# Kernel optimization log

Measured on AMD Instinct MI355X. Metric: run time of the kernel, lower is better.

## Reference

```python
import jax, jax.numpy as jnp
import numpy as np

N_ENTITIES = 100000
D = 128
N_EDGES = 600000
N_RELATIONS = 32
N_USERS = 50000
NNZ = 1000000


def setup_inputs() -> dict:
    key = jax.random.key(0)
    k = jax.random.split(key, 7)
    entity_emb = jax.random.normal(k[0], (N_ENTITIES, D), dtype=jnp.float32)
    edge_index = jax.random.randint(k[1], (2, N_EDGES), 0, N_ENTITIES, dtype=jnp.int64)
    # edge_type in [1, N_RELATIONS] so that weight[edge_type - 1] is in-range
    edge_type = jax.random.randint(k[2], (N_EDGES,), 1, N_RELATIONS + 1, dtype=jnp.int64)
    interact_rows = jax.random.randint(k[3], (NNZ,), 0, N_USERS, dtype=jnp.int64)
    interact_cols = jax.random.randint(k[4], (NNZ,), 0, N_ENTITIES, dtype=jnp.int64)
    interact_vals = jax.random.uniform(k[5], (NNZ,), dtype=jnp.float32)
    weight = jax.random.normal(k[6], (N_RELATIONS, D), dtype=jnp.float32)
    return {
        "entity_emb": entity_emb,
        "edge_index": edge_index,
        "edge_type": edge_type,
        "interact_rows": interact_rows,
        "interact_cols": interact_cols,
        "interact_vals": interact_vals,
        "n_users": N_USERS,
        "weight": weight,
    }


def reference(entity_emb, edge_index, edge_type, interact_rows, interact_cols,
              interact_vals, n_users, weight):
    n_entities = entity_emb.shape[0]
    head, tail = edge_index[0], edge_index[1]

    # KG aggregate: gather -> elementwise mul -> scatter_mean over head
    edge_relation_emb = weight[edge_type - 1]              # [E, D]
    neigh_relation_emb = entity_emb[tail] * edge_relation_emb  # [E, D]
    seg_sum = jax.ops.segment_sum(neigh_relation_emb, head, num_segments=n_entities)
    counts = jax.ops.segment_sum(jnp.ones((head.shape[0],), dtype=entity_emb.dtype),
                                 head, num_segments=n_entities)
    entity_agg = seg_sum / jnp.maximum(counts, 1.0)[:, None]  # mean; empty rows -> 0

    # user aggregate: sparse (COO) @ dense  == segment-sum of scaled gathered rows
    gathered = interact_vals[:, None] * entity_emb[interact_cols]  # [nnz, D]
    user_agg = jax.ops.segment_sum(gathered, interact_rows, num_segments=n_users)

    return entity_agg, user_agg
```

## Files before the change

kernel.cpp:

```cpp
#include <hip/hip_runtime.h>

#define D 128

__device__ __forceinline__ float bf2f(unsigned short u) {
    union { unsigned int i; float f; } v;
    v.i = ((unsigned int)u) << 16;
    return v.f;
}
__device__ __forceinline__ unsigned short f2bf(float f) {
    union { float f; unsigned int i; } v;
    v.f = f;
    unsigned int x = v.i;
    unsigned int round_bit = (x >> 16) & 1u;
    x += 0x7fffu + round_bit;
    return (unsigned short)(x >> 16);
}

__global__ void detect_kernel(const int* __restrict__ et_i32,
                              const unsigned short* __restrict__ emb_u16,
                              int* __restrict__ flags) {
    int lane = threadIdx.x;
    int v = et_i32[2 * lane + 1];
    unsigned long long b_i64 = __ballot(v != 0);

    unsigned short a = emb_u16[2 * lane];
    unsigned short c = emb_u16[2 * lane + 1];
    int e1 = (a >> 7) & 0xFF;
    int e2 = (c >> 7) & 0xFF;
    unsigned long long b_f32 = __ballot(e1 > 140 || e2 > 140);

    if (lane == 0) {
        flags[0] = (b_i64 == 0ULL) ? 1 : 0;
        flags[1] = (b_f32 != 0ULL) ? 1 : 0;
    }
}

__device__ __forceinline__ int idx_at(const void* p, long long i, bool i64) {
    return i64 ? (int)((const long long*)p)[i] : ((const int*)p)[i];
}

__global__ void hist_all(const void* __restrict__ ei, const void* __restrict__ rows,
                         int* __restrict__ cnt, const int* __restrict__ flags,
                         int n_edges, int nnz, int n_entities) {
    long long i = (long long)blockIdx.x * blockDim.x + threadIdx.x;
    bool i64 = flags[0] != 0;
    if (i < n_edges) {
        atomicAdd(&cnt[idx_at(ei, i, i64)], 1);
    } else if (i < (long long)n_edges + nnz) {
        atomicAdd(&cnt[n_entities + idx_at(rows, i - n_edges, i64)], 1);
    }
}

__device__ __forceinline__ int block_scan_excl_256(int v, int* total) {
    __shared__ int tmp[256];
    int tid = threadIdx.x;
    tmp[tid] = v;
    __syncthreads();
    #pragma unroll
    for (int ofs = 1; ofs < 256; ofs <<= 1) {
        int t = (tid >= ofs) ? tmp[tid - ofs] : 0;
        __syncthreads();
        tmp[tid] += t;
        __syncthreads();
    }
    int incl = tmp[tid];
    *total = tmp[255];
    __syncthreads();
    return incl - v;
}

__global__ void scan_p1(const int* __restrict__ cnt, int* __restrict__ bsums, int n) {
    int i = blockIdx.x * 256 + threadIdx.x;
    int v = (i < n) ? cnt[i] : 0;
    int total;
    block_scan_excl_256(v, &total);
    if (threadIdx.x == 0) bsums[blockIdx.x] = total;
}

__global__ void scan_p2(int* __restrict__ bsums, int nb) {
    int tid = threadIdx.x;
    int chunk = (nb + 255) / 256;
    int beg = tid * chunk;
    int end = min(beg + chunk, nb);
    int s = 0;
    for (int i = beg; i < end; ++i) s += bsums[i];
    int total;
    int run = block_scan_excl_256(s, &total);
    for (int i = beg; i < end; ++i) {
        int c = bsums[i];
        bsums[i] = run;
        run += c;
    }
}

__global__ void scan_p3(int* __restrict__ cnt, const int* __restrict__ bsums,
                        int* __restrict__ off, int n) {
    int i = blockIdx.x * 256 + threadIdx.x;
    int v = (i < n) ? cnt[i] : 0;
    int total;
    int excl = block_scan_excl_256(v, &total);
    int base = bsums[blockIdx.x];
    if (i < n) {
        off[i] = base + excl;
        cnt[i] = 0;
        if (i == n - 1) off[n] = base + excl + v;
    }
}

__global__ void scatter_all(const void* __restrict__ ei, const void* __restrict__ et,
                            const void* __restrict__ rows, const void* __restrict__ cols,
                            const void* __restrict__ vals,
                            const int* __restrict__ off, int* __restrict__ cur,
                            int2* __restrict__ pairs, const int* __restrict__ flags,
                            int n_edges, int nnz, int n_entities) {
    long long i = (long long)blockIdx.x * blockDim.x + threadIdx.x;
    bool i64 = flags[0] != 0;
    if (i < n_edges) {
        int head = idx_at(ei, i, i64);
        int tail = idx_at(ei, (long long)n_edges + i, i64);
        int rel  = idx_at(et, i, i64) - 1;
        int pos = off[head] + atomicAdd(&cur[head], 1);
        int2 p; p.x = tail; p.y = rel;
        pairs[pos] = p;
    } else if (i < (long long)n_edges + nnz) {
        long long k = i - n_edges;
        bool f32 = flags[1] != 0;
        int rr = n_entities + idx_at(rows, k, i64);
        int c = idx_at(cols, k, i64);
        float v = f32 ? ((const float*)vals)[k] : bf2f(((const unsigned short*)vals)[k]);
        int pos = off[rr] + atomicAdd(&cur[rr], 1);
        int2 p; p.x = c; p.y = __float_as_int(v);
        pairs[pos] = p;
    }
}

__device__ __forceinline__ void unpack8(uint4 q, float* e) {
    e[0] = bf2f((unsigned short)(q.x & 0xFFFFu)); e[1] = bf2f((unsigned short)(q.x >> 16));
    e[2] = bf2f((unsigned short)(q.y & 0xFFFFu)); e[3] = bf2f((unsigned short)(q.y >> 16));
    e[4] = bf2f((unsigned short)(q.z & 0xFFFFu)); e[5] = bf2f((unsigned short)(q.z >> 16));
    e[6] = bf2f((unsigned short)(q.w & 0xFFFFu)); e[7] = bf2f((unsigned short)(q.w >> 16));
}

__global__ void agg_all(const void* __restrict__ emb, const void* __restrict__ weight,
                        const int* __restrict__ off, const int2* __restrict__ pairs,
                        void* __restrict__ out, const int* __restrict__ flags,
                        int n_entities, int n_total) {
    int gid = blockIdx.x * blockDim.x + threadIdx.x;
    int w = gid >> 6;
    int lane = gid & 63;
    if (w >= n_total) return;
    bool f32 = flags[1] != 0;
    bool isU = (w >= n_entities);
    int m = lane & 15;
    int g = lane >> 4;
    int beg = off[w], end = off[w + 1];

    float acc[8];
    #pragma unroll
    for (int i = 0; i < 8; ++i) acc[i] = 0.f;

    if (!f32) {
        const uint4* embq = (const uint4*)emb;
        if (isU) {
            for (int j = beg + g; j < end; j += 4) {
                int2 p = pairs[j];
                uint4 q = embq[(size_t)p.x * 16 + m];
                float v = __int_as_float(p.y);
                float e[8]; unpack8(q, e);
                #pragma unroll
                for (int i = 0; i < 8; ++i) acc[i] += v * e[i];
            }
        } else {
            const uint4* wq = (const uint4*)weight;
            for (int j = beg + g; j < end; j += 4) {
                int2 p = pairs[j];
                uint4 q  = embq[(size_t)p.x * 16 + m];
                uint4 qw = wq[(size_t)p.y * 16 + m];
                float e[8], wv[8]; unpack8(q, e); unpack8(qw, wv);
                #pragma unroll
                for (int i = 0; i < 8; ++i) acc[i] += e[i] * wv[i];
            }
        }
    } else {
        const float* embf = (const float*)emb;
        if (isU) {
            for (int j = beg + g; j < end; j += 4) {
                int2 p = pairs[j];
                const float4* rp = (const float4*)(embf + (size_t)p.x * D);
                float4 a = rp[m * 2], b = rp[m * 2 + 1];
                float v = __int_as_float(p.y);
                acc[0] += v * a.x; acc[1] += v * a.y; acc[2] += v * a.z; acc[3] += v * a.w;
                acc[4] += v * b.x; acc[5] += v * b.y; acc[6] += v * b.z; acc[7] += v * b.w;
            }
        } else {
            const float* wf = (const float*)weight;
            for (int j = beg + g; j < end; j += 4) {
                int2 p = pairs[j];
                const float4* rp = (const float4*)(embf + (size_t)p.x * D);
                const float4* wp = (const float4*)(wf + (size_t)p.y * D);
                float4 a = rp[m * 2], b = rp[m * 2 + 1];
                float4 wa = wp[m * 2], wb = wp[m * 2 + 1];
                acc[0] += a.x * wa.x; acc[1] += a.y * wa.y; acc[2] += a.z * wa.z; acc[3] += a.w * wa.w;
                acc[4] += b.x * wb.x; acc[5] += b.y * wb.y; acc[6] += b.z * wb.z; acc[7] += b.w * wb.w;
            }
        }
    }

    #pragma unroll
    for (int i = 0; i < 8; ++i) {
        acc[i] += __shfl_xor(acc[i], 16, 64);
        acc[i] += __shfl_xor(acc[i], 32, 64);
    }

    if (!isU) {
        float rcp = 1.0f / fmaxf((float)(end - beg), 1.0f);
        #pragma unroll
        for (int i = 0; i < 8; ++i) acc[i] *= rcp;
    }

    if (g == 0) {
        if (!f32) {
            uint4 o;
            o.x = (unsigned int)f2bf(acc[0]) | ((unsigned int)f2bf(acc[1]) << 16);
            o.y = (unsigned int)f2bf(acc[2]) | ((unsigned int)f2bf(acc[3]) << 16);
            o.z = (unsigned int)f2bf(acc[4]) | ((unsigned int)f2bf(acc[5]) << 16);
            o.w = (unsigned int)f2bf(acc[6]) | ((unsigned int)f2bf(acc[7]) << 16);
            ((uint4*)out)[(size_t)w * 16 + m] = o;
        } else {
            float4* rp = (float4*)((float*)out + (size_t)w * D);
            float4 a, b;
            a.x = acc[0]; a.y = acc[1]; a.z = acc[2]; a.w = acc[3];
            b.x = acc[4]; b.y = acc[5]; b.z = acc[6]; b.w = acc[7];
            rp[m * 2] = a;
            rp[m * 2 + 1] = b;
        }
    }
}

extern "C" void kernel_launch(void* const* d_in, const int* in_sizes, int n_in,
                              void* d_out, int out_size, void* d_ws, size_t ws_size,
                              hipStream_t stream) {
    const void* emb  = d_in[0];
    const void* ei   = d_in[1];
    const void* et   = d_in[2];
    const void* rows = d_in[3];
    const void* cols = d_in[4];
    const void* vals = d_in[5];

    const void* weight = d_in[n_in - 1];
    for (int i = n_in - 1; i >= 5; --i) {
        if (in_sizes[i] >= 256) { weight = d_in[i]; break; }
    }

    int n_entities = in_sizes[0] / D;
    int n_edges    = in_sizes[2];
    int nnz        = in_sizes[5];
    int n_users    = out_size / D - n_entities;

    int n_concat = n_entities + n_users;
    int nb = (n_concat + 255) / 256;

    char* p = (char*)d_ws;
    int2* pairs = (int2*)p;                      p += (size_t)(n_edges + nnz) * sizeof(int2);
    int*  off   = (int*)p;                       p += (size_t)(n_concat + 1) * sizeof(int);
    int*  cnt   = (int*)p;                       p += (size_t)n_concat * sizeof(int);
    int*  bsums = (int*)p;                       p += (size_t)nb * sizeof(int);
    int*  flags = (int*)p;

    (void)hipMemsetAsync(cnt, 0, (size_t)n_concat * sizeof(int), stream);

    const int tpb = 256;

    detect_kernel<<<1, 64, 0, stream>>>((const int*)et, (const unsigned short*)emb, flags);

    {
        long long n = (long long)n_edges + nnz;
        hist_all<<<(int)((n + tpb - 1) / tpb), tpb, 0, stream>>>(
            ei, rows, cnt, flags, n_edges, nnz, n_entities);
    }

    scan_p1<<<nb, 256, 0, stream>>>(cnt, bsums, n_concat);
    scan_p2<<<1, 256, 0, stream>>>(bsums, nb);
    scan_p3<<<nb, 256, 0, stream>>>(cnt, bsums, off, n_concat);

    {
        long long n = (long long)n_edges + nnz;
        scatter_all<<<(int)((n + tpb - 1) / tpb), tpb, 0, stream>>>(
            ei, et, rows, cols, vals, off, cnt, pairs, flags, n_edges, nnz, n_entities);
    }

    {
        long long threads = (long long)n_concat * 64;
        agg_all<<<(int)((threads + tpb - 1) / tpb), tpb, 0, stream>>>(
            emb, weight, off, pairs, d_out, flags, n_entities, n_concat);
    }
}
```

Measured before the change: 408.5 us.

## Record atomic ranks in histogram to skip scatter atomics; shuffle-broadcast pair indices

The histogram pass now keeps each element's destination and the rank returned by its atomicAdd, so the scatter pass writes every pair straight to off[dst]+rank with no second round of atomics. This only happens when the workspace can hold the extra rank array, otherwise the old scatter runs. The f32 aggregation path also loads up to 64 pairs coalesced in one go and broadcasts them with wave shuffles, instead of each lane group reading pairs one at a time. The cost is an extra 8-byte-per-element write and read, plus more branching in the aggregation kernel.

```diff
diff --git a/kernel.cpp b/kernel.cpp
--- a/kernel.cpp
+++ b/kernel.cpp
@@ -40,14 +40,19 @@
 }
 
 __global__ void hist_all(const void* __restrict__ ei, const void* __restrict__ rows,
-                         int* __restrict__ cnt, const int* __restrict__ flags,
+                         int* __restrict__ cnt, int2* __restrict__ dr,
+                         const int* __restrict__ flags,
                          int n_edges, int nnz, int n_entities) {
     long long i = (long long)blockIdx.x * blockDim.x + threadIdx.x;
     bool i64 = flags[0] != 0;
     if (i < n_edges) {
-        atomicAdd(&cnt[idx_at(ei, i, i64)], 1);
+        int dst = idx_at(ei, i, i64);
+        int r = atomicAdd(&cnt[dst], 1);
+        if (dr) { int2 p; p.x = dst; p.y = r; dr[i] = p; }
     } else if (i < (long long)n_edges + nnz) {
-        atomicAdd(&cnt[n_entities + idx_at(rows, i - n_edges, i64)], 1);
+        int dst = n_entities + idx_at(rows, i - n_edges, i64);
+        int r = atomicAdd(&cnt[dst], 1);
+        if (dr) { int2 p; p.x = dst; p.y = r; dr[i] = p; }
     }
 }
 
@@ -104,6 +109,30 @@
         off[i] = base + excl;
         cnt[i] = 0;
         if (i == n - 1) off[n] = base + excl + v;
+    }
+}
+
+__global__ void scatter_rank(const void* __restrict__ ei, const void* __restrict__ et,
+                             const void* __restrict__ cols, const void* __restrict__ vals,
+                             const int* __restrict__ off, const int2* __restrict__ dr,
+                             int2* __restrict__ pairs, const int* __restrict__ flags,
+                             int n_edges, int nnz) {
+    long long i = (long long)blockIdx.x * blockDim.x + threadIdx.x;
+    bool i64 = flags[0] != 0;
+    if (i < n_edges) {
+        int2 d = dr[i];
+        int tail = idx_at(ei, (long long)n_edges + i, i64);
+        int rel  = idx_at(et, i, i64) - 1;
+        int2 p; p.x = tail; p.y = rel;
+        pairs[off[d.x] + d.y] = p;
+    } else if (i < (long long)n_edges + nnz) {
+        long long k = i - n_edges;
+        bool f32 = flags[1] != 0;
+        int2 d = dr[i];
+        int c = idx_at(cols, k, i64);
+        float v = f32 ? ((const float*)vals)[k] : bf2f(((const unsigned short*)vals)[k]);
+        int2 p; p.x = c; p.y = __float_as_int(v);
+        pairs[off[d.x] + d.y] = p;
     }
 }
 
@@ -154,12 +183,60 @@
     int m = lane & 15;
     int g = lane >> 4;
     int beg = off[w], end = off[w + 1];
+    int n = end - beg;
 
     float acc[8];
     #pragma unroll
     for (int i = 0; i < 8; ++i) acc[i] = 0.f;
 
-    if (!f32) {
+    if (f32) {
+        const float4* embq = (const float4*)emb;
+        int nn = min(n, 64);
+        int px = 0, py = 0;
+        if (lane < nn) { int2 t = pairs[beg + lane]; px = t.x; py = t.y; }
+        int TM = (nn + 3) >> 2;
+        if (isU) {
+            for (int t = 0; t < TM; ++t) {
+                int jl = 4 * t + g;
+                int sx = __shfl(px, jl, 64);
+                float v = __int_as_float(__shfl(py, jl, 64));
+                const float4* rp = embq + (size_t)sx * 32 + m * 2;
+                float4 a = rp[0], b = rp[1];
+                acc[0] += v * a.x; acc[1] += v * a.y; acc[2] += v * a.z; acc[3] += v * a.w;
+                acc[4] += v * b.x; acc[5] += v * b.y; acc[6] += v * b.z; acc[7] += v * b.w;
+            }
+            for (int j = beg + 64 + g; j < end; j += 4) {
+                int2 p = pairs[j];
+                float v = __int_as_float(p.y);
+                const float4* rp = embq + (size_t)p.x * 32 + m * 2;
+                float4 a = rp[0], b = rp[1];
+                acc[0] += v * a.x; acc[1] += v * a.y; acc[2] += v * a.z; acc[3] += v * a.w;
+                acc[4] += v * b.x; acc[5] += v * b.y; acc[6] += v * b.z; acc[7] += v * b.w;
+            }
+        } else {
+            const float4* wq = (const float4*)weight;
+            for (int t = 0; t < TM; ++t) {
+                int jl = 4 * t + g;
+                int sx = __shfl(px, jl, 64);
+                int sy = __shfl(py, jl, 64);
+                const float4* rp = embq + (size_t)sx * 32 + m * 2;
+                const float4* wp = wq   + (size_t)sy * 32 + m * 2;
+                float4 a = rp[0], b = rp[1], wa = wp[0], wb = wp[1];
+                if (jl < nn) {
+                    acc[0] += a.x * wa.x; acc[1] += a.y * wa.y; acc[2] += a.z * wa.z; acc[3] += a.w * wa.w;
+                    acc[4] += b.x * wb.x; acc[5] += b.y * wb.y; acc[6] += b.z * wb.z; acc[7] += b.w * wb.w;
+                }
+            }
+            for (int j = beg + 64 + g; j < end; j += 4) {
+                int2 p = pairs[j];
+                const float4* rp = embq + (size_t)p.x * 32 + m * 2;
+                const float4* wp = wq   + (size_t)p.y * 32 + m * 2;
+                float4 a = rp[0], b = rp[1], wa = wp[0], wb = wp[1];
+                acc[0] += a.x * wa.x; acc[1] += a.y * wa.y; acc[2] += a.z * wa.z; acc[3] += a.w * wa.w;
+                acc[4] += b.x * wb.x; acc[5] += b.y * wb.y; acc[6] += b.z * wb.z; acc[7] += b.w * wb.w;
+            }
+        }
+    } else {
         const uint4* embq = (const uint4*)emb;
         if (isU) {
             for (int j = beg + g; j < end; j += 4) {
@@ -179,29 +256,6 @@
                 float e[8], wv[8]; unpack8(q, e); unpack8(qw, wv);
                 #pragma unroll
                 for (int i = 0; i < 8; ++i) acc[i] += e[i] * wv[i];
-            }
-        }
-    } else {
-        const float* embf = (const float*)emb;
-        if (isU) {
-            for (int j = beg + g; j < end; j += 4) {
-                int2 p = pairs[j];
-                const float4* rp = (const float4*)(embf + (size_t)p.x * D);
-                float4 a = rp[m * 2], b = rp[m * 2 + 1];
-                float v = __int_as_float(p.y);
-                acc[0] += v * a.x; acc[1] += v * a.y; acc[2] += v * a.z; acc[3] += v * a.w;
-                acc[4] += v * b.x; acc[5] += v * b.y; acc[6] += v * b.z; acc[7] += v * b.w;
-            }
-        } else {
-            const float* wf = (const float*)weight;
-            for (int j = beg + g; j < end; j += 4) {
-                int2 p = pairs[j];
-                const float4* rp = (const float4*)(embf + (size_t)p.x * D);
-                const float4* wp = (const float4*)(wf + (size_t)p.y * D);
-                float4 a = rp[m * 2], b = rp[m * 2 + 1];
-                float4 wa = wp[m * 2], wb = wp[m * 2 + 1];
-                acc[0] += a.x * wa.x; acc[1] += a.y * wa.y; acc[2] += a.z * wa.z; acc[3] += a.w * wa.w;
-                acc[4] += b.x * wb.x; acc[5] += b.y * wb.y; acc[6] += b.z * wb.z; acc[7] += b.w * wb.w;
             }
         }
     }
@@ -259,9 +313,15 @@
 
     int n_concat = n_entities + n_users;
     int nb = (n_concat + 255) / 256;
+    long long n_pairs = (long long)n_edges + nnz;
+
+    size_t fixed = (size_t)(n_concat + 1 + n_concat + nb + 2) * sizeof(int);
+    bool use_rank = ws_size >= (size_t)n_pairs * sizeof(int2) * 2 + fixed + 256;
 
     char* p = (char*)d_ws;
-    int2* pairs = (int2*)p;                      p += (size_t)(n_edges + nnz) * sizeof(int2);
+    int2* pairs = (int2*)p;                      p += (size_t)n_pairs * sizeof(int2);
+    int2* dr = nullptr;
+    if (use_rank) { dr = (int2*)p;               p += (size_t)n_pairs * sizeof(int2); }
     int*  off   = (int*)p;                       p += (size_t)(n_concat + 1) * sizeof(int);
     int*  cnt   = (int*)p;                       p += (size_t)n_concat * sizeof(int);
     int*  bsums = (int*)p;                       p += (size_t)nb * sizeof(int);
@@ -273,19 +333,18 @@
 
     detect_kernel<<<1, 64, 0, stream>>>((const int*)et, (const unsigned short*)emb, flags);
 
-    {
-        long long n = (long long)n_edges + nnz;
-        hist_all<<<(int)((n + tpb - 1) / tpb), tpb, 0, stream>>>(
-            ei, rows, cnt, flags, n_edges, nnz, n_entities);
-    }
+    hist_all<<<(int)((n_pairs + tpb - 1) / tpb), tpb, 0, stream>>>(
+        ei, rows, cnt, dr, flags, n_edges, nnz, n_entities);
 
     scan_p1<<<nb, 256, 0, stream>>>(cnt, bsums, n_concat);
     scan_p2<<<1, 256, 0, stream>>>(bsums, nb);
     scan_p3<<<nb, 256, 0, stream>>>(cnt, bsums, off, n_concat);
 
-    {
-        long long n = (long long)n_edges + nnz;
-        scatter_all<<<(int)((n + tpb - 1) / tpb), tpb, 0, stream>>>(
+    if (use_rank) {
+        scatter_rank<<<(int)((n_pairs + tpb - 1) / tpb), tpb, 0, stream>>>(
+            ei, et, cols, vals, off, dr, pairs, flags, n_edges, nnz);
+    } else {
+        scatter_all<<<(int)((n_pairs + tpb - 1) / tpb), tpb, 0, stream>>>(
             ei, et, rows, cols, vals, off, cnt, pairs, flags, n_edges, nnz, n_entities);
     }
 
```

After: 356.1 us. -12.8%, faster.
